# Kernel optimization log

Hardware: AMD Instinct MI355X
Metric: run time of the kernel (lower is better)

Reference implementation:

```python
import jax, jax.numpy as jnp
import numpy as np

HEADS = 16
HEAD_DIM = 64


def _attn(q, k, v):
    # q: [..., Q, h, d], k/v: [..., K, h, d]  (non-causal SDPA, scale 1/sqrt(d))
    scale = 1.0 / np.sqrt(HEAD_DIM).astype(np.float32)
    s = jnp.einsum('...qhd,...khd->...hqk', q, k) * scale
    p = jax.nn.softmax(s, axis=-1)
    return jnp.einsum('...hqk,...khd->...qhd', p, v)


def setup_inputs() -> dict:
    key = jax.random.key(0)
    k0, k1, k2 = jax.random.split(key, 3)
    B, T, H, W, D = 4, 32, 16, 16, 1024
    inner = HEADS * HEAD_DIM
    x = jax.random.normal(k0, (B, T, H, W, D), jnp.float32)
    Wqkv = jax.random.normal(k1, (D, 3 * inner), jnp.float32) / np.sqrt(D)
    Wout = jax.random.normal(k2, (inner, D), jnp.float32) / np.sqrt(inner)
    bout = jnp.zeros((D,), jnp.float32)
    return {"x": x, "Wqkv": Wqkv, "Wout": Wout, "bout": bout, "reference_length": 3}


def reference(x, Wqkv, Wout, bout, reference_length):
    B, T, H, W, D = x.shape
    length = reference_length + 1
    n = T // length            # n_frames (chunks)
    S = H * W                  # tokens per frame
    h, d = HEADS, HEAD_DIM

    qkv = jnp.einsum('bthwD,De->bthwe', x, Wqkv)
    q, k, v = jnp.split(qkv, 3, axis=-1)

    def rs(t):  # -> [B, n, length, S, h, d]
        return t.reshape(B, n, length, S, h, d)

    qr, kr, vr = rs(q), rs(k), rs(v)

    # non-last chunks: query = first frame of chunk, keys/values = remaining r frames
    q_pre = qr[:, :-1, 0]                                             # [B, n-1, S, h, d]
    k_pre = kr[:, :-1, 1:].reshape(B, n - 1, reference_length * S, h, d)
    v_pre = vr[:, :-1, 1:].reshape(B, n - 1, reference_length * S, h, d)
    o_pre = _attn(q_pre, k_pre, v_pre).reshape(B, n - 1, H, W, h * d)

    # last chunk: all `length` frames are queries, keys/values = frames 1..length-1
    q_last = qr[:, -1].reshape(B, length * S, h, d)
    k_last = kr[:, -1, 1:].reshape(B, reference_length * S, h, d)
    v_last = vr[:, -1, 1:].reshape(B, reference_length * S, h, d)
    o_last = _attn(q_last, k_last, v_last).reshape(B, length, H, W, h * d)

    o = jnp.concatenate([o_pre, o_last], axis=1)  # [B, n-1+length, H, W, inner]
    return jnp.einsum('bthwe,eD->bthwD', o, Wout) + bout
```

## Files before the change

kernel.cpp:

```cpp
#include <hip/hip_runtime.h>
#include <hip/hip_bf16.h>

typedef __bf16 bf16;
typedef __bf16 bf16x8 __attribute__((ext_vector_type(8)));
typedef float  f32x4  __attribute__((ext_vector_type(4)));
typedef float  f32x4v __attribute__((ext_vector_type(4)));
typedef unsigned int u32x4 __attribute__((ext_vector_type(4)));

#define DEV __device__ __forceinline__

DEV void gload_lds16(const bf16* g, bf16* l) {
    __builtin_amdgcn_global_load_lds(
        (__attribute__((address_space(1))) void*)g,
        (__attribute__((address_space(3))) void*)l, 16, 0, 0);
}

DEV bf16x8 as_bf(u32x4 v) { return __builtin_bit_cast(bf16x8, v); }

DEV f32x4 mfma16(bf16x8 a, bf16x8 b, f32x4 c) {
    return __builtin_amdgcn_mfma_f32_16x16x32_bf16(a, b, c, 0, 0, 0);
}

DEV int cvtpk(float lo, float hi) {
    int r;
    asm("v_cvt_pk_bf16_f32 %0, %1, %2" : "=v"(r) : "v"(lo), "v"(hi));
    return r;
}

constexpr int D_   = 1024;
constexpr int S_   = 256;
constexpr int TOUT = 11;
constexpr int MQ   = 4 * TOUT * S_;
constexpr int MKV  = 4 * 8 * 3 * S_;
constexpr int KVL  = 768;

__global__ void gather_q(const float* __restrict__ x, bf16* __restrict__ Aq) {
    const int idx  = blockIdx.x * 256 + threadIdx.x;
    const int row  = idx >> 7, part = idx & 127;
    const int b    = row / (TOUT * S_);
    const int r2   = row - b * (TOUT * S_);
    const int tout = r2 >> 8;
    const int s    = r2 & 255;
    const int tx   = tout < 7 ? tout * 4 : 28 + (tout - 7);
    const float* src = x + ((size_t)((b * 32 + tx) * S_ + s)) * D_ + part * 8;
    f32x4v v0 = *(const f32x4v*)src;
    f32x4v v1 = *(const f32x4v*)(src + 4);
    bf16x8 o;
    o[0]=(bf16)v0[0]; o[1]=(bf16)v0[1]; o[2]=(bf16)v0[2]; o[3]=(bf16)v0[3];
    o[4]=(bf16)v1[0]; o[5]=(bf16)v1[1]; o[6]=(bf16)v1[2]; o[7]=(bf16)v1[3];
    *(bf16x8*)(Aq + (size_t)row * D_ + part * 8) = o;
}

__global__ void gather_kv(const float* __restrict__ x, bf16* __restrict__ Akv) {
    const int idx = blockIdx.x * 256 + threadIdx.x;
    const int row = idx >> 7, part = idx & 127;
    const int b   = row / 6144;
    const int r2  = row - b * 6144;
    const int c   = r2 / KVL;
    const int j   = r2 - c * KVL;
    const int f   = 1 + (j >> 8);
    const int s   = j & 255;
    const int tx  = c * 4 + f;
    const float* src = x + ((size_t)((b * 32 + tx) * S_ + s)) * D_ + part * 8;
    f32x4v v0 = *(const f32x4v*)src;
    f32x4v v1 = *(const f32x4v*)(src + 4);
    bf16x8 o;
    o[0]=(bf16)v0[0]; o[1]=(bf16)v0[1]; o[2]=(bf16)v0[2]; o[3]=(bf16)v0[3];
    o[4]=(bf16)v1[0]; o[5]=(bf16)v1[1]; o[6]=(bf16)v1[2]; o[7]=(bf16)v1[3];
    *(bf16x8*)(Akv + (size_t)row * D_ + part * 8) = o;
}

__global__ void wtrans(const float* __restrict__ W, bf16* __restrict__ Wt, int N) {
    __shared__ float T[64][65];
    const int bid = blockIdx.x;
    const int kt = bid & 15, nt = bid >> 4;
    const int k0 = kt * 64, n0 = nt * 64;
    for (int i = 0; i < 16; ++i) {
        const int e = i * 256 + (int)threadIdx.x;
        const int kk = e >> 6, nn = e & 63;
        T[nn][kk] = W[(size_t)(k0 + kk) * N + n0 + nn];
    }
    __syncthreads();
    for (int i = 0; i < 16; ++i) {
        const int e = i * 256 + (int)threadIdx.x;
        const int n = e >> 6, kk = e & 63;
        Wt[(size_t)(n0 + n) * 1024 + k0 + kk] = (bf16)T[n][kk];
    }
}

__global__ void vtrans(const bf16* __restrict__ KV, bf16* __restrict__ Vt) {
    __shared__ bf16 T[64][66];
    const int bid = blockIdx.x;
    const int jt = bid % 12;
    const int h  = (bid / 12) & 15;
    const int bg = bid / 192;
    const int j0 = jt * 64;
    const bf16* src = KV + (size_t)bg * KVL * 2048 + 1024 + h * 64;
    for (int i = 0; i < 16; ++i) {
        const int e = i * 256 + (int)threadIdx.x;
        const int j = e >> 6, dd = e & 63;
        T[dd][j] = src[(size_t)(j0 + j) * 2048 + dd];
    }
    __syncthreads();
    bf16* dst = Vt + ((size_t)(bg * 16 + h)) * 64 * KVL;
    for (int i = 0; i < 16; ++i) {
        const int e = i * 256 + (int)threadIdx.x;
        const int d = e >> 6, jj = e & 63;
        dst[(size_t)d * KVL + j0 + jj] = T[d][jj];
    }
}

#define PH_MID() do { \
    __builtin_amdgcn_s_barrier(); \
    asm volatile("s_waitcnt lgkmcnt(0)" ::: "memory"); \
    __builtin_amdgcn_sched_barrier(0); \
    __builtin_amdgcn_s_setprio(1); \
} while(0)

#define PH_END() do { \
    __builtin_amdgcn_s_setprio(0); \
    __builtin_amdgcn_sched_barrier(0); \
    __builtin_amdgcn_s_barrier(); \
} while(0)

#define VM6() asm volatile("s_waitcnt vmcnt(6)" ::: "memory")

#define STAGE_A(bufc, half, tile) do { \
    const bf16* s0_ = pA + (size_t)(half) * 64 * 1024 + (tile) * 64; \
    bf16* d0_ = ldsA + (bufc) * 16384 + (half) * 8192; \
    gload_lds16(s0_, d0_); \
    gload_lds16(s0_ + (size_t)128 * 1024, d0_ + 4096); \
} while(0)

#define STAGE_B(bufc, half, tile) do { \
    const bf16* s0_ = pB + (size_t)(half) * 32 * 1024 + (tile) * 64; \
    bf16* d0_ = ldsB + (bufc) * 16384 + (half) * 8192; \
    gload_lds16(s0_, d0_); \
    gload_lds16(s0_ + (size_t)128 * 1024, d0_ + 4096); \
} while(0)

#define LDA(bufc, mh) do { \
    const bf16* p_ = sm + (bufc) * 16384 + (mh) * 8192; \
    _Pragma("unroll") \
    for (int j_ = 0; j_ < 4; ++j_) { \
        a[j_][0] = *(const u32x4*)(p_ + j_ * 1024 + eA0); \
        a[j_][1] = *(const u32x4*)(p_ + j_ * 1024 + eA1); \
    } \
} while(0)

#define LDB(bufc, nh) do { \
    const bf16* p_ = sm + 32768 + (bufc) * 16384 + (nh) * 8192; \
    _Pragma("unroll") \
    for (int j_ = 0; j_ < 2; ++j_) { \
        b[(nh)*2 + j_][0] = *(const u32x4*)(p_ + j_ * 1024 + eB0); \
        b[(nh)*2 + j_][1] = *(const u32x4*)(p_ + j_ * 1024 + eB1); \
    } \
} while(0)

#define MM(mh, nh) do { \
    _Pragma("unroll") \
    for (int j_ = 0; j_ < 4; ++j_) { \
        _Pragma("unroll") \
        for (int i_ = 0; i_ < 2; ++i_) { \
            f32x4 c_ = acc[(mh)*4 + j_][(nh)*2 + i_]; \
            c_ = mfma16(as_bf(a[j_][0]), as_bf(b[(nh)*2 + i_][0]), c_); \
            c_ = mfma16(as_bf(a[j_][1]), as_bf(b[(nh)*2 + i_][1]), c_); \
            acc[(mh)*4 + j_][(nh)*2 + i_] = c_; \
        } \
    } \
} while(0)

template<int EPI>
__global__ __launch_bounds__(512) void gemm8(
    const bf16* __restrict__ A, const bf16* __restrict__ Bt,
    bf16* __restrict__ Cb, float* __restrict__ Cf,
    const float* __restrict__ bias, int N, int mt, int nwg)
{
    __shared__ bf16 sm[65536];
    const int tid = threadIdx.x, lane = tid & 63, wid = tid >> 6;

    int wg = blockIdx.x;
    {
        const int q = nwg >> 3, r = nwg & 7, xcd = wg & 7, off = wg >> 3;
        wg = (xcd < r ? xcd * (q + 1) : r * (q + 1) + (xcd - r) * q) + off;
    }
    const int bm = wg % mt, bn = wg / mt;
    const int wr = wid >> 2, wc = wid & 3;
    const int l15 = lane & 15, l4 = lane >> 4;

    const int Rrow = (wid << 3) + (lane >> 3);
    const int G    = (lane & 7) ^ (lane >> 3);
    const bf16* pA = A  + (size_t)(bm * 256 + Rrow) * 1024 + G * 8;
    const int wc1 = Rrow >> 5, cc1 = Rrow & 31;
    const bf16* pB = Bt + (size_t)(bn * 256 + wc1 * 64 + cc1) * 1024 + G * 8;
    bf16* ldsA = sm + (wid << 9);
    bf16* ldsB = sm + 32768 + (wid << 9);

    const int g0  = l4 ^ (l15 & 7);
    const int eA0 = wr * 4096 + l15 * 64 + g0 * 8;
    const int eA1 = eA0 ^ 32;
    const int eB0 = wc * 2048 + l15 * 64 + g0 * 8;
    const int eB1 = eB0 ^ 32;

    f32x4 acc[8][4];
    u32x4 a[4][2], b[4][2];
    const f32x4 zf = {0.f, 0.f, 0.f, 0.f};
    #pragma unroll
    for (int m = 0; m < 8; ++m)
        #pragma unroll
        for (int n = 0; n < 4; ++n) acc[m][n] = zf;

    STAGE_A(0, 0, 0); STAGE_B(0, 0, 0); STAGE_B(0, 1, 0); STAGE_A(0, 1, 0);
    STAGE_A(1, 0, 1); STAGE_B(1, 0, 1); STAGE_B(1, 1, 1);
    asm volatile("s_waitcnt vmcnt(6)" ::: "memory");
    __builtin_amdgcn_s_barrier();

    #pragma unroll 1
    for (int t = 0; t < 8; ++t) {
        const int T1 = 2 * t + 1;
        const int n0 = (2 * t + 2 < 15) ? 2 * t + 2 : 15;
        const int n1 = (2 * t + 3 < 15) ? 2 * t + 3 : 15;
        LDA(0, 0); LDB(0, 0); STAGE_A(1, 1, T1);
        PH_MID(); MM(0, 0); PH_END();
        LDB(0, 1); STAGE_A(0, 0, n0);
        PH_MID(); MM(0, 1); PH_END();
        LDA(0, 1); STAGE_B(0, 0, n0);
        PH_MID(); MM(1, 0); PH_END();
        STAGE_B(0, 1, n0);
        PH_MID(); MM(1, 1); VM6(); PH_END();
        LDA(1, 0); LDB(1, 0); STAGE_A(0, 1, n0);
        PH_MID(); MM(0, 0); PH_END();
        LDB(1, 1); STAGE_A(1, 0, n1);
        PH_MID(); MM(0, 1); PH_END();
        LDA(1, 1); STAGE_B(1, 0, n1);
        PH_MID(); MM(1, 0); PH_END();
        STAGE_B(1, 1, n1);
        PH_MID(); MM(1, 1); VM6(); PH_END();
    }
    asm volatile("s_waitcnt vmcnt(0)" ::: "memory");

    #pragma unroll
    for (int m = 0; m < 8; ++m) {
        const int row = bm * 256 + wr * 128 + m * 16 + l4 * 4;
        #pragma unroll
        for (int n = 0; n < 4; ++n) {
            const int col = bn * 256 + wc * 64 + n * 16 + l15;
            f32x4 v = acc[m][n];
            if (EPI == 0) {
                #pragma unroll
                for (int r = 0; r < 4; ++r)
                    Cb[(size_t)(row + r) * N + col] = (bf16)v[r];
            } else {
                const float bs = bias[col];
                #pragma unroll
                for (int r = 0; r < 4; ++r)
                    Cf[(size_t)(row + r) * N + col] = v[r] + bs;
            }
        }
    }
}

__global__ __launch_bounds__(256, 4) void attn_fwd(
    const bf16* __restrict__ Q, const bf16* __restrict__ KV,
    const bf16* __restrict__ Vt, bf16* __restrict__ O)
{
    __shared__ bf16 Kl[2][2][64][32];
    __shared__ bf16 Vl[2][2][64][32];

    const int tid = threadIdx.x, lane = tid & 63, wid = tid >> 6;
    int bid = blockIdx.x;
    const int h = bid & 15; bid >>= 4;
    const int qt = bid % 44, b = bid / 44;
    const int chunk = qt < 28 ? (qt >> 2) : 7;
    const int qrow0 = b * (TOUT * S_) +
                      (qt < 28 ? chunk * S_ + (qt & 3) * 64 : 7 * S_ + (qt - 28) * 64);

    const bf16* kg = KV + ((size_t)(b * 8 + chunk) * KVL) * 2048 + h * 64;
    const bf16* vg = Vt + ((size_t)((b * 8 + chunk) * 16 + h)) * 64 * KVL;

    const int l15 = lane & 15, l4 = lane >> 4;

    const bf16* qp = Q + (size_t)(qrow0 + wid * 16 + l15) * D_ + h * 64 + l4 * 8;
    u32x4 q0, q1;
    {
        bf16x8 t0 = *(const bf16x8*)qp;
        bf16x8 t1 = *(const bf16x8*)(qp + 32);
        #pragma unroll
        for (int j = 0; j < 8; ++j) {
            t0[j] = (bf16)((float)t0[j] * 0.125f);
            t1[j] = (bf16)((float)t1[j] * 0.125f);
        }
        q0 = __builtin_bit_cast(u32x4, t0);
        q1 = __builtin_bit_cast(u32x4, t1);
    }

    const int R   = wid * 16 + (lane >> 2);
    const int gsw = ((lane & 3) ^ ((lane >> 3) & 3)) * 8;
    const int rg  = (l4 ^ ((l15 >> 1) & 3)) * 8;

    const int baseA = ((2 * (l4 & 1)) * 16 + l15) * 4;
    const int baseB = baseA + 64;
    const bool hi2 = (l4 & 2) != 0;

    float m_s = -1e30f, l_s = 0.f;
    f32x4 oacc[4];
    const f32x4 zf = {0.f, 0.f, 0.f, 0.f};
    #pragma unroll
    for (int m2 = 0; m2 < 4; ++m2) oacc[m2] = zf;

#define ASTAGE(c, t) do { \
    const int kv0_ = (t) * 64; \
    gload_lds16(kg + (size_t)(kv0_ + R) * 2048 + gsw,      &Kl[c][0][0][0] + wid * 512); \
    gload_lds16(kg + (size_t)(kv0_ + R) * 2048 + 32 + gsw, &Kl[c][1][0][0] + wid * 512); \
    gload_lds16(vg + (size_t)R * KVL + kv0_ + gsw,         &Vl[c][0][0][0] + wid * 512); \
    gload_lds16(vg + (size_t)R * KVL + kv0_ + 32 + gsw,    &Vl[c][1][0][0] + wid * 512); \
} while (0)

    ASTAGE(0, 0);
    __syncthreads();

    #pragma unroll 1
    for (int kt = 0; kt < 12; ++kt) {
        const int cur = kt & 1;
        if (kt < 11) ASTAGE(cur ^ 1, kt + 1);

        f32x4 s[4];
        #pragma unroll
        for (int n = 0; n < 4; ++n) {
            const bf16* kp = &Kl[cur][0][n * 16 + l15][0] + rg;
            const u32x4 k0 = *(const u32x4*)kp;
            const u32x4 k1 = *(const u32x4*)(kp + 2048);
            f32x4 t = mfma16(as_bf(k0), as_bf(q0), zf);
            s[n] = mfma16(as_bf(k1), as_bf(q1), t);
        }

        float pm = s[0][0];
        #pragma unroll
        for (int n = 0; n < 4; ++n)
            #pragma unroll
            for (int r = 0; r < 4; ++r) pm = fmaxf(pm, s[n][r]);
        pm = fmaxf(pm, __shfl_xor(pm, 16));
        pm = fmaxf(pm, __shfl_xor(pm, 32));
        const float mn = fmaxf(m_s, pm);
        const float al = __expf(m_s - mn);
        m_s = mn;
        float p[4][4];
        float sum = 0.f;
        #pragma unroll
        for (int n = 0; n < 4; ++n)
            #pragma unroll
            for (int r = 0; r < 4; ++r) {
                const float e = __expf(s[n][r] - mn);
                p[n][r] = e; sum += e;
            }
        sum += __shfl_xor(sum, 16);
        sum += __shfl_xor(sum, 32);
        l_s = l_s * al + sum;
        #pragma unroll
        for (int m2 = 0; m2 < 4; ++m2) oacc[m2] *= al;

        int u[4][2];
        #pragma unroll
        for (int n = 0; n < 4; ++n) {
            u[n][0] = cvtpk(p[n][0], p[n][1]);
            u[n][1] = cvtpk(p[n][2], p[n][3]);
        }

        #pragma unroll
        for (int kk = 0; kk < 2; ++kk) {
            const int e0 = __builtin_amdgcn_ds_bpermute(baseA, u[2 * kk][0]);
            const int f0 = __builtin_amdgcn_ds_bpermute(baseA, u[2 * kk + 1][0]);
            const int e1 = __builtin_amdgcn_ds_bpermute(baseA, u[2 * kk][1]);
            const int f1 = __builtin_amdgcn_ds_bpermute(baseA, u[2 * kk + 1][1]);
            const int e2 = __builtin_amdgcn_ds_bpermute(baseB, u[2 * kk][0]);
            const int f2 = __builtin_amdgcn_ds_bpermute(baseB, u[2 * kk + 1][0]);
            const int e3 = __builtin_amdgcn_ds_bpermute(baseB, u[2 * kk][1]);
            const int f3 = __builtin_amdgcn_ds_bpermute(baseB, u[2 * kk + 1][1]);
            u32x4 pb;
            pb[0] = (unsigned)(hi2 ? f0 : e0);
            pb[1] = (unsigned)(hi2 ? f1 : e1);
            pb[2] = (unsigned)(hi2 ? f2 : e2);
            pb[3] = (unsigned)(hi2 ? f3 : e3);
            #pragma unroll
            for (int m2 = 0; m2 < 4; ++m2) {
                const u32x4 vf = *(const u32x4*)(&Vl[cur][kk][m2 * 16 + l15][0] + rg);
                oacc[m2] = mfma16(as_bf(vf), as_bf(pb), oacc[m2]);
            }
        }
        __syncthreads();
    }
#undef ASTAGE

    const float inv = 1.f / l_s;
    bf16* sc = &Kl[0][0][0][0] + wid * 1152;
    #pragma unroll
    for (int m2 = 0; m2 < 4; ++m2)
        #pragma unroll
        for (int r = 0; r < 4; ++r)
            sc[l15 * 72 + m2 * 16 + l4 * 4 + r] = (bf16)(oacc[m2][r] * inv);
    const int rq = lane >> 2, rd = (lane & 3) * 16;
    const bf16* sr = sc + rq * 72 + rd;
    const u32x4 o0 = *(const u32x4*)sr;
    const u32x4 o1 = *(const u32x4*)(sr + 8);
    bf16* op = O + (size_t)(qrow0 + wid * 16 + rq) * D_ + h * 64 + rd;
    *(u32x4*)op = o0;
    *(u32x4*)(op + 8) = o1;
}

extern "C" void kernel_launch(void* const* d_in, const int* in_sizes, int n_in,
                              void* d_out, int out_size, void* d_ws, size_t ws_size,
                              hipStream_t stream) {
    (void)in_sizes; (void)n_in; (void)out_size; (void)ws_size;
    const float* x    = (const float*)d_in[0];
    const float* Wqkv = (const float*)d_in[1];
    const float* Wout = (const float*)d_in[2];
    const float* bout = (const float*)d_in[3];

    bf16* Aq     = (bf16*)d_ws;
    bf16* Akv    = Aq     + (size_t)MQ  * 1024;
    bf16* Wqkv_t = Akv    + (size_t)MKV * 1024;
    bf16* Wout_t = Wqkv_t + (size_t)3072 * 1024;
    bf16* Qb     = Wout_t + (size_t)1024 * 1024;
    bf16* KVb    = Qb     + (size_t)MQ  * 1024;
    bf16* Vtb    = Akv;
    bf16* Ob     = Aq;

    gather_q <<<MQ  * 128 / 256, 256, 0, stream>>>(x, Aq);
    gather_kv<<<MKV * 128 / 256, 256, 0, stream>>>(x, Akv);
    wtrans<<<16 * 48, 256, 0, stream>>>(Wqkv, Wqkv_t, 3072);
    wtrans<<<16 * 16, 256, 0, stream>>>(Wout, Wout_t, 1024);

    gemm8<0><<<176, 512, 0, stream>>>(Aq, Wqkv_t, Qb, nullptr, nullptr,
                                      1024, 44, 176);
    gemm8<0><<<768, 512, 0, stream>>>(Akv, Wqkv_t + (size_t)1024 * 1024, KVb,
                                      nullptr, nullptr, 2048, 96, 768);

    vtrans<<<32 * 16 * 12, 256, 0, stream>>>(KVb, Vtb);
    attn_fwd<<<4 * 44 * 16, 256, 0, stream>>>(Qb, KVb, Vtb, Ob);

    gemm8<1><<<176, 512, 0, stream>>>(Ob, Wout_t, nullptr, (float*)d_out, bout,
                                      1024, 44, 176);
}
```

Before: 316.2 us.

## Merge prep kernels, fuse Q and KV GEMMs, write V transposed in epilogue

The four gather and weight-transpose kernels are merged into one prep launch. The Q and KV projection GEMMs are merged into a single launch with 944 workgroups, and the separate vtrans kernel is removed by having the V-column tiles write their output already transposed from the GEMM epilogue. K is now stored with a 1024 stride, and attention reads it accordingly. This cuts the number of launches and one full round trip of V through memory, at the cost of narrow 8-byte strided stores in the V epilogue and a hardcoded XCD remap.

```diff
diff --git a/kernel.cpp b/kernel.cpp
--- a/kernel.cpp
+++ b/kernel.cpp
@@ -6,6 +6,7 @@
 typedef float  f32x4  __attribute__((ext_vector_type(4)));
 typedef float  f32x4v __attribute__((ext_vector_type(4)));
 typedef unsigned int u32x4 __attribute__((ext_vector_type(4)));
+typedef unsigned short u16x4 __attribute__((ext_vector_type(4)));
 
 #define DEV __device__ __forceinline__
 
@@ -34,80 +35,75 @@
 constexpr int MKV  = 4 * 8 * 3 * S_;
 constexpr int KVL  = 768;
 
-__global__ void gather_q(const float* __restrict__ x, bf16* __restrict__ Aq) {
-    const int idx  = blockIdx.x * 256 + threadIdx.x;
-    const int row  = idx >> 7, part = idx & 127;
-    const int b    = row / (TOUT * S_);
-    const int r2   = row - b * (TOUT * S_);
-    const int tout = r2 >> 8;
-    const int s    = r2 & 255;
-    const int tx   = tout < 7 ? tout * 4 : 28 + (tout - 7);
-    const float* src = x + ((size_t)((b * 32 + tx) * S_ + s)) * D_ + part * 8;
+constexpr int PB_WQKV = 768;
+constexpr int PB_WOUT = 256;
+constexpr int PB_GQ   = MQ  * 128 / 256;
+constexpr int PB_GKV  = MKV * 128 / 256;
+constexpr int PB_TOT  = PB_WQKV + PB_WOUT + PB_GQ + PB_GKV;
+
+__global__ void prep(const float* __restrict__ x,
+                     const float* __restrict__ Wqkv,
+                     const float* __restrict__ Wout,
+                     bf16* __restrict__ Aq, bf16* __restrict__ Akv,
+                     bf16* __restrict__ Wqkv_t, bf16* __restrict__ Wout_t)
+{
+    __shared__ float T[64][65];
+    const int tid = threadIdx.x;
+    int wg = blockIdx.x;
+
+    if (wg < PB_WQKV + PB_WOUT) {
+        const float* W; bf16* Wt; int N, bid2;
+        if (wg < PB_WQKV) { W = Wqkv; Wt = Wqkv_t; N = 3072; bid2 = wg; }
+        else              { W = Wout; Wt = Wout_t; N = 1024; bid2 = wg - PB_WQKV; }
+        const int kt = bid2 & 15, nt = bid2 >> 4;
+        const int k0 = kt * 64, n0 = nt * 64;
+        for (int i = 0; i < 16; ++i) {
+            const int e = i * 256 + tid;
+            const int kk = e >> 6, nn = e & 63;
+            T[nn][kk] = W[(size_t)(k0 + kk) * N + n0 + nn];
+        }
+        __syncthreads();
+        for (int i = 0; i < 16; ++i) {
+            const int e = i * 256 + tid;
+            const int n = e >> 6, kk = e & 63;
+            Wt[(size_t)(n0 + n) * 1024 + k0 + kk] = (bf16)T[n][kk];
+        }
+        return;
+    }
+    wg -= PB_WQKV + PB_WOUT;
+
+    int row, part;
+    const float* src;
+    bf16* dst;
+    if (wg < PB_GQ) {
+        const int idx = wg * 256 + tid;
+        row = idx >> 7; part = idx & 127;
+        const int b    = row / (TOUT * S_);
+        const int r2   = row - b * (TOUT * S_);
+        const int tout = r2 >> 8;
+        const int s    = r2 & 255;
+        const int tx   = tout < 7 ? tout * 4 : 28 + (tout - 7);
+        src = x + ((size_t)((b * 32 + tx) * S_ + s)) * D_ + part * 8;
+        dst = Aq + (size_t)row * D_ + part * 8;
+    } else {
+        const int idx = (wg - PB_GQ) * 256 + tid;
+        row = idx >> 7; part = idx & 127;
+        const int b  = row / 6144;
+        const int r2 = row - b * 6144;
+        const int c  = r2 / KVL;
+        const int j  = r2 - c * KVL;
+        const int f  = 1 + (j >> 8);
+        const int s  = j & 255;
+        const int tx = c * 4 + f;
+        src = x + ((size_t)((b * 32 + tx) * S_ + s)) * D_ + part * 8;
+        dst = Akv + (size_t)row * D_ + part * 8;
+    }
     f32x4v v0 = *(const f32x4v*)src;
     f32x4v v1 = *(const f32x4v*)(src + 4);
     bf16x8 o;
     o[0]=(bf16)v0[0]; o[1]=(bf16)v0[1]; o[2]=(bf16)v0[2]; o[3]=(bf16)v0[3];
     o[4]=(bf16)v1[0]; o[5]=(bf16)v1[1]; o[6]=(bf16)v1[2]; o[7]=(bf16)v1[3];
-    *(bf16x8*)(Aq + (size_t)row * D_ + part * 8) = o;
-}
-
-__global__ void gather_kv(const float* __restrict__ x, bf16* __restrict__ Akv) {
-    const int idx = blockIdx.x * 256 + threadIdx.x;
-    const int row = idx >> 7, part = idx & 127;
-    const int b   = row / 6144;
-    const int r2  = row - b * 6144;
-    const int c   = r2 / KVL;
-    const int j   = r2 - c * KVL;
-    const int f   = 1 + (j >> 8);
-    const int s   = j & 255;
-    const int tx  = c * 4 + f;
-    const float* src = x + ((size_t)((b * 32 + tx) * S_ + s)) * D_ + part * 8;
-    f32x4v v0 = *(const f32x4v*)src;
-    f32x4v v1 = *(const f32x4v*)(src + 4);
-    bf16x8 o;
-    o[0]=(bf16)v0[0]; o[1]=(bf16)v0[1]; o[2]=(bf16)v0[2]; o[3]=(bf16)v0[3];
-    o[4]=(bf16)v1[0]; o[5]=(bf16)v1[1]; o[6]=(bf16)v1[2]; o[7]=(bf16)v1[3];
-    *(bf16x8*)(Akv + (size_t)row * D_ + part * 8) = o;
-}
-
-__global__ void wtrans(const float* __restrict__ W, bf16* __restrict__ Wt, int N) {
-    __shared__ float T[64][65];
-    const int bid = blockIdx.x;
-    const int kt = bid & 15, nt = bid >> 4;
-    const int k0 = kt * 64, n0 = nt * 64;
-    for (int i = 0; i < 16; ++i) {
-        const int e = i * 256 + (int)threadIdx.x;
-        const int kk = e >> 6, nn = e & 63;
-        T[nn][kk] = W[(size_t)(k0 + kk) * N + n0 + nn];
-    }
-    __syncthreads();
-    for (int i = 0; i < 16; ++i) {
-        const int e = i * 256 + (int)threadIdx.x;
-        const int n = e >> 6, kk = e & 63;
-        Wt[(size_t)(n0 + n) * 1024 + k0 + kk] = (bf16)T[n][kk];
-    }
-}
-
-__global__ void vtrans(const bf16* __restrict__ KV, bf16* __restrict__ Vt) {
-    __shared__ bf16 T[64][66];
-    const int bid = blockIdx.x;
-    const int jt = bid % 12;
-    const int h  = (bid / 12) & 15;
-    const int bg = bid / 192;
-    const int j0 = jt * 64;
-    const bf16* src = KV + (size_t)bg * KVL * 2048 + 1024 + h * 64;
-    for (int i = 0; i < 16; ++i) {
-        const int e = i * 256 + (int)threadIdx.x;
-        const int j = e >> 6, dd = e & 63;
-        T[dd][j] = src[(size_t)(j0 + j) * 2048 + dd];
-    }
-    __syncthreads();
-    bf16* dst = Vt + ((size_t)(bg * 16 + h)) * 64 * KVL;
-    for (int i = 0; i < 16; ++i) {
-        const int e = i * 256 + (int)threadIdx.x;
-        const int d = e >> 6, jj = e & 63;
-        dst[(size_t)d * KVL + j0 + jj] = T[d][jj];
-    }
+    *(bf16x8*)dst = o;
 }
 
 #define PH_MID() do { \
@@ -170,21 +166,54 @@
     } \
 } while(0)
 
-template<int EPI>
-__global__ __launch_bounds__(512) void gemm8(
-    const bf16* __restrict__ A, const bf16* __restrict__ Bt,
-    bf16* __restrict__ Cb, float* __restrict__ Cf,
-    const float* __restrict__ bias, int N, int mt, int nwg)
+#define GEMM_MAINLOOP() \
+    STAGE_A(0, 0, 0); STAGE_B(0, 0, 0); STAGE_B(0, 1, 0); STAGE_A(0, 1, 0); \
+    STAGE_A(1, 0, 1); STAGE_B(1, 0, 1); STAGE_B(1, 1, 1); \
+    asm volatile("s_waitcnt vmcnt(6)" ::: "memory"); \
+    __builtin_amdgcn_s_barrier(); \
+    _Pragma("unroll 1") \
+    for (int t = 0; t < 8; ++t) { \
+        const int T1 = 2 * t + 1; \
+        const int n0 = (2 * t + 2 < 15) ? 2 * t + 2 : 15; \
+        const int n1 = (2 * t + 3 < 15) ? 2 * t + 3 : 15; \
+        LDA(0, 0); LDB(0, 0); STAGE_A(1, 1, T1); \
+        PH_MID(); MM(0, 0); PH_END(); \
+        LDB(0, 1); STAGE_A(0, 0, n0); \
+        PH_MID(); MM(0, 1); PH_END(); \
+        LDA(0, 1); STAGE_B(0, 0, n0); \
+        PH_MID(); MM(1, 0); PH_END(); \
+        STAGE_B(0, 1, n0); \
+        PH_MID(); MM(1, 1); VM6(); PH_END(); \
+        LDA(1, 0); LDB(1, 0); STAGE_A(0, 1, n0); \
+        PH_MID(); MM(0, 0); PH_END(); \
+        LDB(1, 1); STAGE_A(1, 0, n1); \
+        PH_MID(); MM(0, 1); PH_END(); \
+        LDA(1, 1); STAGE_B(1, 0, n1); \
+        PH_MID(); MM(1, 0); PH_END(); \
+        STAGE_B(1, 1, n1); \
+        PH_MID(); MM(1, 1); VM6(); PH_END(); \
+    } \
+    asm volatile("s_waitcnt vmcnt(0)" ::: "memory")
+
+__global__ __launch_bounds__(512) void gemm_qkv(
+    const bf16* __restrict__ Aq, const bf16* __restrict__ Akv,
+    const bf16* __restrict__ Wt,
+    bf16* __restrict__ Qb, bf16* __restrict__ Kb, bf16* __restrict__ Vt)
 {
     __shared__ bf16 sm[65536];
     const int tid = threadIdx.x, lane = tid & 63, wid = tid >> 6;
 
     int wg = blockIdx.x;
     {
-        const int q = nwg >> 3, r = nwg & 7, xcd = wg & 7, off = wg >> 3;
-        wg = (xcd < r ? xcd * (q + 1) : r * (q + 1) + (xcd - r) * q) + off;
-    }
-    const int bm = wg % mt, bn = wg / mt;
+        const int xcd = wg & 7, off = wg >> 3;
+        wg = xcd * 118 + off;
+    }
+    const bool isQ = wg < 176;
+    const bf16* A;  const bf16* Bt;  int bm, bn;
+    if (isQ) { A = Aq;  Bt = Wt;                      bm = wg % 44;  bn = wg / 44; }
+    else     { wg -= 176;
+               A = Akv; Bt = Wt + (size_t)1024 * 1024; bm = wg % 96;  bn = wg / 96; }
+
     const int wr = wid >> 2, wc = wid & 3;
     const int l15 = lane & 15, l4 = lane >> 4;
 
@@ -210,34 +239,83 @@
         #pragma unroll
         for (int n = 0; n < 4; ++n) acc[m][n] = zf;
 
-    STAGE_A(0, 0, 0); STAGE_B(0, 0, 0); STAGE_B(0, 1, 0); STAGE_A(0, 1, 0);
-    STAGE_A(1, 0, 1); STAGE_B(1, 0, 1); STAGE_B(1, 1, 1);
-    asm volatile("s_waitcnt vmcnt(6)" ::: "memory");
-    __builtin_amdgcn_s_barrier();
-
-    #pragma unroll 1
-    for (int t = 0; t < 8; ++t) {
-        const int T1 = 2 * t + 1;
-        const int n0 = (2 * t + 2 < 15) ? 2 * t + 2 : 15;
-        const int n1 = (2 * t + 3 < 15) ? 2 * t + 3 : 15;
-        LDA(0, 0); LDB(0, 0); STAGE_A(1, 1, T1);
-        PH_MID(); MM(0, 0); PH_END();
-        LDB(0, 1); STAGE_A(0, 0, n0);
-        PH_MID(); MM(0, 1); PH_END();
-        LDA(0, 1); STAGE_B(0, 0, n0);
-        PH_MID(); MM(1, 0); PH_END();
-        STAGE_B(0, 1, n0);
-        PH_MID(); MM(1, 1); VM6(); PH_END();
-        LDA(1, 0); LDB(1, 0); STAGE_A(0, 1, n0);
-        PH_MID(); MM(0, 0); PH_END();
-        LDB(1, 1); STAGE_A(1, 0, n1);
-        PH_MID(); MM(0, 1); PH_END();
-        LDA(1, 1); STAGE_B(1, 0, n1);
-        PH_MID(); MM(1, 0); PH_END();
-        STAGE_B(1, 1, n1);
-        PH_MID(); MM(1, 1); VM6(); PH_END();
-    }
-    asm volatile("s_waitcnt vmcnt(0)" ::: "memory");
+    GEMM_MAINLOOP();
+
+    if (isQ || bn < 4) {
+        bf16* C = isQ ? Qb : Kb;
+        #pragma unroll
+        for (int m = 0; m < 8; ++m) {
+            const int row = bm * 256 + wr * 128 + m * 16 + l4 * 4;
+            #pragma unroll
+            for (int n = 0; n < 4; ++n) {
+                const int col = bn * 256 + wc * 64 + n * 16 + l15;
+                f32x4 v = acc[m][n];
+                #pragma unroll
+                for (int r = 0; r < 4; ++r)
+                    C[(size_t)(row + r) * 1024 + col] = (bf16)v[r];
+            }
+        }
+    } else {
+        const int vb = bm / 3;
+        const int j0base = (bm % 3) * 256;
+        #pragma unroll
+        for (int m = 0; m < 8; ++m) {
+            const int j0 = j0base + wr * 128 + m * 16 + l4 * 4;
+            #pragma unroll
+            for (int n = 0; n < 4; ++n) {
+                const int colv = (bn - 4) * 256 + wc * 64 + n * 16 + l15;
+                f32x4 v = acc[m][n];
+                u16x4 pk;
+                #pragma unroll
+                for (int r = 0; r < 4; ++r) {
+                    bf16 t = (bf16)v[r];
+                    pk[r] = __builtin_bit_cast(unsigned short, t);
+                }
+                *(u16x4*)(Vt + ((size_t)vb * 1024 + colv) * KVL + j0) = pk;
+            }
+        }
+    }
+}
+
+__global__ __launch_bounds__(512) void gemm_out(
+    const bf16* __restrict__ A, const bf16* __restrict__ Bt,
+    float* __restrict__ Cf, const float* __restrict__ bias)
+{
+    __shared__ bf16 sm[65536];
+    const int tid = threadIdx.x, lane = tid & 63, wid = tid >> 6;
+
+    int wg = blockIdx.x;
+    {
+        const int xcd = wg & 7, off = wg >> 3;
+        wg = xcd * 22 + off;
+    }
+    const int bm = wg % 44, bn = wg / 44;
+    const int wr = wid >> 2, wc = wid & 3;
+    const int l15 = lane & 15, l4 = lane >> 4;
+
+    const int Rrow = (wid << 3) + (lane >> 3);
+    const int G    = (lane & 7) ^ (lane >> 3);
+    const bf16* pA = A  + (size_t)(bm * 256 + Rrow) * 1024 + G * 8;
+    const int wc1 = Rrow >> 5, cc1 = Rrow & 31;
+    const bf16* pB = Bt + (size_t)(bn * 256 + wc1 * 64 + cc1) * 1024 + G * 8;
+    bf16* ldsA = sm + (wid << 9);
+    bf16* ldsB = sm + 32768 + (wid << 9);
+
+    const int g0  = l4 ^ (l15 & 7);
+    const int eA0 = wr * 4096 + l15 * 64 + g0 * 8;
+    const int eA1 = eA0 ^ 32;
+    const int eB0 = wc * 2048 + l15 * 64 + g0 * 8;
+    const int eB1 = eB0 ^ 32;
+
+    f32x4 acc[8][4];
+    u32x4 a[4][2], b[4][2];
+    const f32x4 zf = {0.f, 0.f, 0.f, 0.f};
+    #pragma unroll
+    for (int m = 0; m < 8; ++m)
+        #pragma unroll
+        for (int n = 0; n < 4; ++n) acc[m][n] = zf;
+
+    GEMM_MAINLOOP();
 
     #pragma unroll
     for (int m = 0; m < 8; ++m) {
@@ -246,22 +324,16 @@
         for (int n = 0; n < 4; ++n) {
             const int col = bn * 256 + wc * 64 + n * 16 + l15;
             f32x4 v = acc[m][n];
-            if (EPI == 0) {
-                #pragma unroll
-                for (int r = 0; r < 4; ++r)
-                    Cb[(size_t)(row + r) * N + col] = (bf16)v[r];
-            } else {
-                const float bs = bias[col];
-                #pragma unroll
-                for (int r = 0; r < 4; ++r)
-                    Cf[(size_t)(row + r) * N + col] = v[r] + bs;
-            }
+            const float bs = bias[col];
+            #pragma unroll
+            for (int r = 0; r < 4; ++r)
+                Cf[(size_t)(row + r) * 1024 + col] = v[r] + bs;
         }
     }
 }
 
 __global__ __launch_bounds__(256, 4) void attn_fwd(
-    const bf16* __restrict__ Q, const bf16* __restrict__ KV,
+    const bf16* __restrict__ Q, const bf16* __restrict__ K,
     const bf16* __restrict__ Vt, bf16* __restrict__ O)
 {
     __shared__ bf16 Kl[2][2][64][32];
@@ -275,7 +347,7 @@
     const int qrow0 = b * (TOUT * S_) +
                       (qt < 28 ? chunk * S_ + (qt & 3) * 64 : 7 * S_ + (qt - 28) * 64);
 
-    const bf16* kg = KV + ((size_t)(b * 8 + chunk) * KVL) * 2048 + h * 64;
+    const bf16* kg = K  + ((size_t)(b * 8 + chunk) * KVL) * 1024 + h * 64;
     const bf16* vg = Vt + ((size_t)((b * 8 + chunk) * 16 + h)) * 64 * KVL;
 
     const int l15 = lane & 15, l4 = lane >> 4;
@@ -310,8 +382,8 @@
 
 #define ASTAGE(c, t) do { \
     const int kv0_ = (t) * 64; \
-    gload_lds16(kg + (size_t)(kv0_ + R) * 2048 + gsw,      &Kl[c][0][0][0] + wid * 512); \
-    gload_lds16(kg + (size_t)(kv0_ + R) * 2048 + 32 + gsw, &Kl[c][1][0][0] + wid * 512); \
+    gload_lds16(kg + (size_t)(kv0_ + R) * 1024 + gsw,      &Kl[c][0][0][0] + wid * 512); \
+    gload_lds16(kg + (size_t)(kv0_ + R) * 1024 + 32 + gsw, &Kl[c][1][0][0] + wid * 512); \
     gload_lds16(vg + (size_t)R * KVL + kv0_ + gsw,         &Vl[c][0][0][0] + wid * 512); \
     gload_lds16(vg + (size_t)R * KVL + kv0_ + 32 + gsw,    &Vl[c][1][0][0] + wid * 512); \
 } while (0)
@@ -421,23 +493,15 @@
     bf16* Wqkv_t = Akv    + (size_t)MKV * 1024;
     bf16* Wout_t = Wqkv_t + (size_t)3072 * 1024;
     bf16* Qb     = Wout_t + (size_t)1024 * 1024;
-    bf16* KVb    = Qb     + (size_t)MQ  * 1024;
-    bf16* Vtb    = Akv;
+    bf16* Kb     = Qb     + (size_t)MQ  * 1024;
+    bf16* Vtb    = Kb     + (size_t)MKV * 1024;
     bf16* Ob     = Aq;
 
-    gather_q <<<MQ  * 128 / 256, 256, 0, stream>>>(x, Aq);
-    gather_kv<<<MKV * 128 / 256, 256, 0, stream>>>(x, Akv);
-    wtrans<<<16 * 48, 256, 0, stream>>>(Wqkv, Wqkv_t, 3072);
-    wtrans<<<16 * 16, 256, 0, stream>>>(Wout, Wout_t, 1024);
-
-    gemm8<0><<<176, 512, 0, stream>>>(Aq, Wqkv_t, Qb, nullptr, nullptr,
-                                      1024, 44, 176);
-    gemm8<0><<<768, 512, 0, stream>>>(Akv, Wqkv_t + (size_t)1024 * 1024, KVb,
-                                      nullptr, nullptr, 2048, 96, 768);
-
-    vtrans<<<32 * 16 * 12, 256, 0, stream>>>(KVb, Vtb);
-    attn_fwd<<<4 * 44 * 16, 256, 0, stream>>>(Qb, KVb, Vtb, Ob);
-
-    gemm8<1><<<176, 512, 0, stream>>>(Ob, Wout_t, nullptr, (float*)d_out, bout,
-                                      1024, 44, 176);
-}
+    prep<<<PB_TOT, 256, 0, stream>>>(x, Wqkv, Wout, Aq, Akv, Wqkv_t, Wout_t);
+
+    gemm_qkv<<<944, 512, 0, stream>>>(Aq, Akv, Wqkv_t, Qb, Kb, Vtb);
+
+    attn_fwd<<<4 * 44 * 16, 256, 0, stream>>>(Qb, Kb, Vtb, Ob);
+
+    gemm_out<<<176, 512, 0, stream>>>(Ob, Wout_t, (float*)d_out, bout);
+}
```

New measurement: 308.4 us. -2.5%, faster.
